# Optimization experiments

Hardware: AMD Instinct MI355X
Metric: run time of the kernel (lower is better)

The kernel has to match this reference:

```python
import jax, jax.numpy as jnp
import numpy as np

B, N, E = 2, 10000, 160000
NODE_DIM, EDGE_DIM, HIDDEN = 128, 64, 256


def setup_inputs() -> dict:
    key = jax.random.key(0)
    ks = jax.random.split(key, 12)
    def lin(k, fan_in, fan_out):
        return jax.random.normal(k, (fan_in, fan_out), dtype=jnp.float32) / np.sqrt(fan_in)
    msg_in = 2 * NODE_DIM + EDGE_DIM   # 320
    upd_in = NODE_DIM + HIDDEN         # 384
    return {
        "node_features": jax.random.normal(ks[0], (B, N, NODE_DIM), dtype=jnp.float32),
        "edge_indices": jax.random.randint(ks[1], (B, E, 2), 0, N, dtype=jnp.int32),
        "edge_features": jax.random.normal(ks[2], (B, E, EDGE_DIM), dtype=jnp.float32),
        "W1m": lin(ks[3], msg_in, HIDDEN),  "b1m": jnp.zeros((HIDDEN,), jnp.float32),
        "W2m": lin(ks[4], HIDDEN, HIDDEN),  "b2m": jnp.zeros((HIDDEN,), jnp.float32),
        "W1u": lin(ks[5], upd_in, HIDDEN),  "b1u": jnp.zeros((HIDDEN,), jnp.float32),
        "W2u": lin(ks[6], HIDDEN, NODE_DIM), "b2u": jnp.zeros((NODE_DIM,), jnp.float32),
    }


def reference(node_features, edge_indices, edge_features,
              W1m, b1m, W2m, b2m, W1u, b1u, W2u, b2u):
    # node_features: [B, N, D]; edge_indices: [B, E, 2]; edge_features: [B, E, F]
    b, n, d = node_features.shape
    e = edge_indices.shape[1]
    src_idx = edge_indices[..., 0]  # [B, E]
    dst_idx = edge_indices[..., 1]  # [B, E]
    # batched gather of endpoint features
    src = jnp.take_along_axis(node_features, src_idx[..., None], axis=1)  # [B, E, D]
    dst = jnp.take_along_axis(node_features, dst_idx[..., None], axis=1)  # [B, E, D]
    msg_in = jnp.concatenate([src, dst, edge_features], axis=-1)          # [B, E, 2D+F]
    h = jax.nn.gelu(jnp.einsum("bei,ih->beh", msg_in, W1m) + b1m)
    messages = jnp.einsum("beh,ho->beo", h, W2m) + b2m                    # [B, E, H]
    # scatter-add into destination node buckets (flatten batch for segment_sum)
    flat_dst = (dst_idx + (jnp.arange(b, dtype=dst_idx.dtype)[:, None] * n)).reshape(-1)
    aggregated = jax.ops.segment_sum(
        messages.reshape(b * e, -1), flat_dst, num_segments=b * n
    ).reshape(b, n, -1)                                                   # [B, N, H]
    upd_in = jnp.concatenate([node_features, aggregated], axis=-1)        # [B, N, D+H]
    u = jax.nn.gelu(jnp.einsum("bni,ih->bnh", upd_in, W1u) + b1u)
    return jnp.einsum("bnh,ho->bno", u, W2u) + b2u                        # [B, N, D]
```

## Files before the change

kernel.cpp:

```cpp
#include <hip/hip_runtime.h>
#include <hip/hip_bf16.h>
#include <math.h>

#define BATCH   2
#define N_NODES 10000
#define E_EDGES 160000
#define BN      (BATCH * N_NODES)
#define BE      (BATCH * E_EDGES)
#define ND      128
#define ED      64
#define HID     256
#define K1      320
#define K2      256
#define K1U     384
#define NOUT    128
#define TMN     32
#define TME     64
#define LDH     264

typedef __attribute__((ext_vector_type(8))) short bf16x8;
typedef __attribute__((ext_vector_type(4))) float f32x4;

__device__ unsigned short g_Pb[(size_t)BN * 512];
__device__ unsigned short g_nodef_bf[(size_t)BN * ND];
__device__ unsigned short g_w1c[HID * K1U];
__device__ unsigned short g_w2ut[K2 * NOUT];
__device__ float          g_bc[HID];
__device__ int            g_hist[BN];

__device__ __forceinline__ float gelu_tanh(float x) {
    float u = 0.7978845608028654f * (x + 0.044715f * x * x * x);
    float e = __expf(2.0f * u);
    float t = 1.0f - 2.0f * __builtin_amdgcn_rcpf(e + 1.0f);
    return 0.5f * x * (1.0f + t);
}

__device__ __forceinline__ unsigned short f2bf(float f) {
    __hip_bfloat16 h = __float2bfloat16(f);
    return *reinterpret_cast<unsigned short*>(&h);
}

__device__ __forceinline__ float bf2f(unsigned short u) {
    unsigned int x = ((unsigned int)u) << 16;
    return *reinterpret_cast<float*>(&x);
}

__global__ __launch_bounds__(256) void prep_all(
    const float* __restrict__ nodef,
    const float* __restrict__ W1m, unsigned short* __restrict__ w1t,
    const float* __restrict__ W1u, const float* __restrict__ W2u,
    const float* __restrict__ W2m, const float* __restrict__ b2m)
{
    int i = blockIdx.x * blockDim.x + threadIdx.x;
    if (i < BN * ND / 4) {
        float4 v = ((const float4*)nodef)[i];
        ushort4 o;
        o.x = f2bf(v.x); o.y = f2bf(v.y); o.z = f2bf(v.z); o.w = f2bf(v.w);
        ((ushort4*)g_nodef_bf)[i] = o;
    }
    if (i < BN) g_hist[i] = 0;
    if (i < K1 * HID) {
        int k = i % K1, n = i / K1;
        w1t[i] = f2bf(W1m[(size_t)k * HID + n]);
    }
    if (i < ND * HID) {
        int k = i % ND, n = i / ND;
        g_w1c[n * K1U + k] = f2bf(W1u[(size_t)k * HID + n]);
    }
    if (i < K2 * NOUT) {
        int k = i % K2, n = i / K2;
        g_w2ut[i] = f2bf(W2u[(size_t)k * NOUT + n]);
    }
    if (i < HID * HID) {
        int n = i & 255;
        int j = i >> 8;
        float a = 0.f;
        #pragma unroll 8
        for (int o = 0; o < HID; ++o)
            a += W2m[(size_t)j * HID + o] * W1u[(size_t)(128 + o) * HID + n];
        g_w1c[n * K1U + 128 + j] = f2bf(a);
    }
    if (i < HID) {
        float c = 0.f;
        #pragma unroll 8
        for (int o = 0; o < HID; ++o)
            c += b2m[o] * W1u[(size_t)(128 + o) * HID + i];
        g_bc[i] = c;
    }
}

__global__ __launch_bounds__(256) void dst_hist(
    const int* __restrict__ eidx, float* __restrict__ agg)
{
    int e = blockIdx.x * blockDim.x + threadIdx.x;
    float4 z = {0.f, 0.f, 0.f, 0.f};
    #pragma unroll
    for (int j = 0; j < 4; ++j)
        ((float4*)agg)[(size_t)j * BE + e] = z;
    if (e < BE) {
        int dst = eidx[2 * e + 1];
        int b   = e / E_EDGES;
        atomicAdd(&g_hist[b * N_NODES + dst], 1);
    }
}

__global__ __launch_bounds__(1024, 1) void scan20k(int* __restrict__ offs)
{
    __shared__ int sh[BN];
    __shared__ int tots[1024];
    const int tid = threadIdx.x;
    for (int j = tid; j < BN; j += 1024) sh[j] = g_hist[j];
    __syncthreads();
    const int base = tid * 20;
    int v[20];
    int s = 0;
    #pragma unroll
    for (int j = 0; j < 20; ++j) {
        int i = base + j;
        int h = (i < BN) ? sh[i] : 0;
        v[j] = s; s += h;
    }
    tots[tid] = s;
    __syncthreads();
    #pragma unroll
    for (int d = 1; d < 1024; d <<= 1) {
        int t = (tid >= d) ? tots[tid - d] : 0;
        __syncthreads();
        tots[tid] += t;
        __syncthreads();
    }
    int excl = tots[tid] - s;
    #pragma unroll
    for (int j = 0; j < 20; ++j) {
        int i = base + j;
        if (i < BN) sh[i] = excl + v[j];
    }
    __syncthreads();
    for (int j = tid; j < BN; j += 1024) offs[j] = sh[j];
}

__global__ __launch_bounds__(512, 2) void pgemm_scatter(
    const unsigned short* __restrict__ w1t,
    const int* __restrict__ eidx,
    int* __restrict__ offs, int* __restrict__ perm)
{
    const int tid  = threadIdx.x;
    {
        int e   = blockIdx.x * 512 + tid;
        int2 se = ((const int2*)eidx)[e];
        int b   = (e >= E_EDGES) ? 1 : 0;
        int pos = atomicAdd(&offs[b * N_NODES + se.y], 1);
        perm[pos] = e;
    }

    const int wave = tid >> 6;
    const int lane = tid & 63;
    const int quad = lane >> 4;
    const int r16  = lane & 15;
    const int n0   = blockIdx.x * TMN;

    const int jb   = (wave & 3) * 64;
    const int koff = (wave < 4) ? 0 : 128;
    const int cb   = (wave < 4) ? 0 : 256;

    f32x4 acc[2][4];
    #pragma unroll
    for (int mt = 0; mt < 2; ++mt)
        #pragma unroll
        for (int nt = 0; nt < 4; ++nt)
            acc[mt][nt] = (f32x4){0.f, 0.f, 0.f, 0.f};

    for (int ks = 0; ks < ND / 32; ++ks) {
        bf16x8 wf[4], nf[2];
        #pragma unroll
        for (int nt = 0; nt < 4; ++nt)
            wf[nt] = *(const bf16x8*)&w1t[(size_t)(jb + nt * 16 + r16) * K1
                                          + koff + ks * 32 + quad * 8];
        #pragma unroll
        for (int mt = 0; mt < 2; ++mt)
            nf[mt] = *(const bf16x8*)&g_nodef_bf[(size_t)(n0 + mt * 16 + r16) * ND
                                                 + ks * 32 + quad * 8];
        #pragma unroll
        for (int mt = 0; mt < 2; ++mt)
            #pragma unroll
            for (int nt = 0; nt < 4; ++nt)
                acc[mt][nt] = __builtin_amdgcn_mfma_f32_16x16x32_bf16(
                    wf[nt], nf[mt], acc[mt][nt], 0, 0, 0);
    }

    #pragma unroll
    for (int nt = 0; nt < 4; ++nt) {
        int j0 = cb + jb + nt * 16 + quad * 4;
        #pragma unroll
        for (int mt = 0; mt < 2; ++mt) {
            int m = n0 + mt * 16 + r16;
            ushort4 o;
            o.x = f2bf(acc[mt][nt][0]); o.y = f2bf(acc[mt][nt][1]);
            o.z = f2bf(acc[mt][nt][2]); o.w = f2bf(acc[mt][nt][3]);
            *(ushort4*)&g_Pb[(size_t)m * 512 + j0] = o;
        }
    }
}

#define EK_SE   0
#define EK_SH   8192
#define EK_SMEM (8192 + TME * LDH * 2)

__global__ __launch_bounds__(512, 6) void edge_mlp_mfma(
    const int*            __restrict__ eidx,
    const float*          __restrict__ edgef,
    const int*            __restrict__ perm,
    const unsigned short* __restrict__ w1t,
    const float*          __restrict__ b1m,
    float* __restrict__ agg)
{
    __shared__ __align__(16) char smem[EK_SMEM];
    unsigned short* sE = (unsigned short*)(smem + EK_SE);
    unsigned short* sH = (unsigned short*)(smem + EK_SH);
    __shared__ int s_src[TME];
    __shared__ int s_dst[TME];
    __shared__ int s_eid[TME];

    const int tid  = threadIdx.x;
    const int wave = tid >> 6;
    const int lane = tid & 63;
    const int quad = lane >> 4;
    const int r16  = lane & 15;
    const int be0  = blockIdx.x * TME;

    if (tid < TME) {
        int eid = perm[be0 + tid];
        int b   = eid / E_EDGES;
        int2 se = ((const int2*)eidx)[eid];
        s_eid[tid] = eid;
        s_src[tid] = b * N_NODES + se.x;
        s_dst[tid] = b * N_NODES + se.y;
    }

    const unsigned short* wB1 = w1t + (size_t)(wave * 32) * K1 + 256;
    bf16x8 wf00 = *(const bf16x8*)&wB1[(size_t)r16        * K1 + quad * 8];
    bf16x8 wf01 = *(const bf16x8*)&wB1[(size_t)r16        * K1 + 32 + quad * 8];
    bf16x8 wf10 = *(const bf16x8*)&wB1[(size_t)(16 + r16) * K1 + quad * 8];
    bf16x8 wf11 = *(const bf16x8*)&wB1[(size_t)(16 + r16) * K1 + 32 + quad * 8];

    __syncthreads();

    {
        int row = tid >> 3;
        int c0  = (tid & 7) * 8;
        const float* fp = edgef + (size_t)s_eid[row] * ED + c0;
        float4 v0 = *(const float4*)fp;
        float4 v1 = *(const float4*)(fp + 4);
        ushort4 o0, o1;
        o0.x = f2bf(v0.x); o0.y = f2bf(v0.y); o0.z = f2bf(v0.z); o0.w = f2bf(v0.w);
        o1.x = f2bf(v1.x); o1.y = f2bf(v1.y); o1.z = f2bf(v1.z); o1.w = f2bf(v1.w);
        int p2 = c0 >> 5, kk = c0 & 31;
        *(ushort4*)&sE[p2 * 2048 + row * 32 + kk]     = o0;
        *(ushort4*)&sE[p2 * 2048 + row * 32 + kk + 4] = o1;
    }
    __syncthreads();

    f32x4 acc[4][2];
    #pragma unroll
    for (int mt = 0; mt < 4; ++mt)
        #pragma unroll
        for (int nt = 0; nt < 2; ++nt)
            acc[mt][nt] = (f32x4){0.f, 0.f, 0.f, 0.f};

    #pragma unroll
    for (int mt = 0; mt < 4; ++mt) {
        bf16x8 e0 = *(const bf16x8*)&sE[(mt * 16 + r16) * 32 + quad * 8];
        bf16x8 e1 = *(const bf16x8*)&sE[2048 + (mt * 16 + r16) * 32 + quad * 8];
        acc[mt][0] = __builtin_amdgcn_mfma_f32_16x16x32_bf16(wf00, e0, acc[mt][0], 0, 0, 0);
        acc[mt][1] = __builtin_amdgcn_mfma_f32_16x16x32_bf16(wf10, e0, acc[mt][1], 0, 0, 0);
        acc[mt][0] = __builtin_amdgcn_mfma_f32_16x16x32_bf16(wf01, e1, acc[mt][0], 0, 0, 0);
        acc[mt][1] = __builtin_amdgcn_mfma_f32_16x16x32_bf16(wf11, e1, acc[mt][1], 0, 0, 0);
    }

    {
        float4 bb[2];
        bb[0] = *(const float4*)&b1m[wave * 32 + quad * 4];
        bb[1] = *(const float4*)&b1m[wave * 32 + 16 + quad * 4];
        #pragma unroll
        for (int mt = 0; mt < 4; ++mt) {
            int m = mt * 16 + r16;
            const unsigned short* pS = &g_Pb[(size_t)s_src[m] * 512];
            const unsigned short* pD = &g_Pb[(size_t)s_dst[m] * 512 + 256];
            #pragma unroll
            for (int nt = 0; nt < 2; ++nt) {
                int n0 = wave * 32 + nt * 16 + quad * 4;
                ushort4 us = *(const ushort4*)(pS + n0);
                ushort4 ud = *(const ushort4*)(pD + n0);
                ushort4 o;
                o.x = f2bf(gelu_tanh(acc[mt][nt][0] + bf2f(us.x) + bf2f(ud.x) + bb[nt].x));
                o.y = f2bf(gelu_tanh(acc[mt][nt][1] + bf2f(us.y) + bf2f(ud.y) + bb[nt].y));
                o.z = f2bf(gelu_tanh(acc[mt][nt][2] + bf2f(us.z) + bf2f(ud.z) + bb[nt].z));
                o.w = f2bf(gelu_tanh(acc[mt][nt][3] + bf2f(us.w) + bf2f(ud.w) + bb[nt].w));
                *(ushort4*)&sH[m * LDH + n0] = o;
            }
        }
    }
    __syncthreads();

    {
        const int cc = tid & 255;
        const int r0 = (tid >> 8) * 32;
        int   cur  = s_dst[r0];
        float racc = 0.f;
        for (int mb = 0; mb < 32; mb += 8) {
            float v[8];
            #pragma unroll
            for (int j = 0; j < 8; ++j)
                v[j] = bf2f(sH[(r0 + mb + j) * LDH + cc]);
            #pragma unroll
            for (int j = 0; j < 8; ++j) {
                int d = s_dst[r0 + mb + j];
                if (d != cur) {
                    atomicAdd(&agg[(size_t)cur * HID + cc], racc);
                    cur = d; racc = v[j];
                } else {
                    racc += v[j];
                }
            }
        }
        atomicAdd(&agg[(size_t)cur * HID + cc], racc);
    }
}

__global__ __launch_bounds__(256, 4) void node_mlp_mfma(
    const float* __restrict__ agg,
    const float* __restrict__ b1u,
    const float* __restrict__ b2u,
    float* __restrict__ out)
{
    __shared__ __align__(16) unsigned short sH[TMN * LDH];

    const int tid  = threadIdx.x;
    const int wave = tid >> 6;
    const int lane = tid & 63;
    const int quad = lane >> 4;
    const int r16  = lane & 15;
    const int n0   = blockIdx.x * TMN;

    f32x4 acc[2][4];
    #pragma unroll
    for (int mt = 0; mt < 2; ++mt)
        #pragma unroll
        for (int nt = 0; nt < 4; ++nt)
            acc[mt][nt] = (f32x4){0.f, 0.f, 0.f, 0.f};

    for (int ks = 0; ks < 4; ++ks) {
        bf16x8 wf[4], nf[2];
        #pragma unroll
        for (int nt = 0; nt < 4; ++nt)
            wf[nt] = *(const bf16x8*)&g_w1c[(size_t)(wave * 64 + nt * 16 + r16) * K1U
                                            + ks * 32 + quad * 8];
        #pragma unroll
        for (int mt = 0; mt < 2; ++mt)
            nf[mt] = *(const bf16x8*)&g_nodef_bf[(size_t)(n0 + mt * 16 + r16) * ND
                                                 + ks * 32 + quad * 8];
        #pragma unroll
        for (int mt = 0; mt < 2; ++mt)
            #pragma unroll
            for (int nt = 0; nt < 4; ++nt)
                acc[mt][nt] = __builtin_amdgcn_mfma_f32_16x16x32_bf16(
                    wf[nt], nf[mt], acc[mt][nt], 0, 0, 0);
    }
    for (int ks = 0; ks < 8; ++ks) {
        bf16x8 wf[4], nf[2];
        #pragma unroll
        for (int nt = 0; nt < 4; ++nt)
            wf[nt] = *(const bf16x8*)&g_w1c[(size_t)(wave * 64 + nt * 16 + r16) * K1U
                                            + (4 + ks) * 32 + quad * 8];
        #pragma unroll
        for (int mt = 0; mt < 2; ++mt) {
            const float* fp = &agg[(size_t)(n0 + mt * 16 + r16) * HID + ks * 32 + quad * 8];
            float4 v0 = *(const float4*)fp;
            float4 v1 = *(const float4*)(fp + 4);
            union { bf16x8 v; ushort4 u[2]; } cv;
            cv.u[0] = (ushort4){f2bf(v0.x), f2bf(v0.y), f2bf(v0.z), f2bf(v0.w)};
            cv.u[1] = (ushort4){f2bf(v1.x), f2bf(v1.y), f2bf(v1.z), f2bf(v1.w)};
            nf[mt] = cv.v;
        }
        #pragma unroll
        for (int mt = 0; mt < 2; ++mt)
            #pragma unroll
            for (int nt = 0; nt < 4; ++nt)
                acc[mt][nt] = __builtin_amdgcn_mfma_f32_16x16x32_bf16(
                    wf[nt], nf[mt], acc[mt][nt], 0, 0, 0);
    }

    #pragma unroll
    for (int nt = 0; nt < 4; ++nt) {
        int nn0 = wave * 64 + nt * 16 + quad * 4;
        float4 bb = *(const float4*)&b1u[nn0];
        float4 bc = *(const float4*)&g_bc[nn0];
        #pragma unroll
        for (int mt = 0; mt < 2; ++mt) {
            int row = n0 + mt * 16 + r16;
            float hv = (float)g_hist[row];
            int m = mt * 16 + r16;
            ushort4 o;
            o.x = f2bf(gelu_tanh(acc[mt][nt][0] + bb.x + hv * bc.x));
            o.y = f2bf(gelu_tanh(acc[mt][nt][1] + bb.y + hv * bc.y));
            o.z = f2bf(gelu_tanh(acc[mt][nt][2] + bb.z + hv * bc.z));
            o.w = f2bf(gelu_tanh(acc[mt][nt][3] + bb.w + hv * bc.w));
            *(ushort4*)&sH[m * LDH + nn0] = o;
        }
    }
    __syncthreads();

    f32x4 acc2[2][2];
    #pragma unroll
    for (int mt = 0; mt < 2; ++mt)
        #pragma unroll
        for (int nt = 0; nt < 2; ++nt)
            acc2[mt][nt] = (f32x4){0.f, 0.f, 0.f, 0.f};

    for (int ks = 0; ks < K2 / 32; ++ks) {
        bf16x8 wf2[2], hf[2];
        #pragma unroll
        for (int nt = 0; nt < 2; ++nt)
            wf2[nt] = *(const bf16x8*)&g_w2ut[(size_t)(wave * 32 + nt * 16 + r16) * K2
                                              + ks * 32 + quad * 8];
        #pragma unroll
        for (int mt = 0; mt < 2; ++mt)
            hf[mt] = *(const bf16x8*)&sH[(mt * 16 + r16) * LDH + ks * 32 + quad * 8];
        #pragma unroll
        for (int mt = 0; mt < 2; ++mt)
            #pragma unroll
            for (int nt = 0; nt < 2; ++nt)
                acc2[mt][nt] = __builtin_amdgcn_mfma_f32_16x16x32_bf16(
                    wf2[nt], hf[mt], acc2[mt][nt], 0, 0, 0);
    }

    #pragma unroll
    for (int nt = 0; nt < 2; ++nt) {
        int j0 = wave * 32 + nt * 16 + quad * 4;
        float4 bb = *(const float4*)&b2u[j0];
        #pragma unroll
        for (int mt = 0; mt < 2; ++mt) {
            int row = n0 + mt * 16 + r16;
            float4 v = {acc2[mt][nt][0] + bb.x, acc2[mt][nt][1] + bb.y,
                        acc2[mt][nt][2] + bb.z, acc2[mt][nt][3] + bb.w};
            *(float4*)&out[(size_t)row * NOUT + j0] = v;
        }
    }
}


extern "C" void kernel_launch(void* const* d_in, const int* in_sizes, int n_in,
                              void* d_out, int out_size, void* d_ws, size_t ws_size,
                              hipStream_t stream) {
    const float* nodef = (const float*)d_in[0];
    const int*   eidx  = (const int*)  d_in[1];
    const float* edgef = (const float*)d_in[2];
    const float* W1m   = (const float*)d_in[3];
    const float* b1m   = (const float*)d_in[4];
    const float* W2m   = (const float*)d_in[5];
    const float* b2m   = (const float*)d_in[6];
    const float* W1u   = (const float*)d_in[7];
    const float* b1u   = (const float*)d_in[8];
    const float* W2u   = (const float*)d_in[9];
    const float* b2u   = (const float*)d_in[10];
    float* out = (float*)d_out;

    char* wsb = (char*)d_ws;
    float* agg = (float*)wsb;

    char* ob = (char*)d_out;
    unsigned short* w1t  = (unsigned short*)(ob + 5120000);
    int* offs            = (int*)(ob + 5494912);
    int* perm            = (int*)(ob + 5574912);

    prep_all<<<(BN * ND / 4 + 255) / 256, 256, 0, stream>>>(
        nodef, W1m, w1t, W1u, W2u, W2m, b2m);

    dst_hist<<<BE / 256, 256, 0, stream>>>(eidx, agg);
    scan20k<<<1, 1024, 0, stream>>>(offs);

    pgemm_scatter<<<BN / TMN, 512, 0, stream>>>(w1t, eidx, offs, perm);

    edge_mlp_mfma<<<BE / TME, 512, 0, stream>>>(
        eidx, edgef, perm, w1t, b1m, agg);

    node_mlp_mfma<<<BN / TMN, 256, 0, stream>>>(agg, b1u, b2u, out);
}
```

Before: 340.3 us.

## Fuse histogram into prep kernel and alias edge-kernel LDS buffers

Result: faster. 331.5 us (-2.6%).

```diff
diff --git a/kernel.cpp b/kernel.cpp
--- a/kernel.cpp
+++ b/kernel.cpp
@@ -27,6 +27,7 @@
 __device__ unsigned short g_w2ut[K2 * NOUT];
 __device__ float          g_bc[HID];
 __device__ int            g_hist[BN];
+__device__ int            g_offs[BN];
 
 __device__ __forceinline__ float gelu_tanh(float x) {
     float u = 0.7978845608028654f * (x + 0.044715f * x * x * x);
@@ -45,20 +46,30 @@
     return *reinterpret_cast<float*>(&x);
 }
 
-__global__ __launch_bounds__(256) void prep_all(
-    const float* __restrict__ nodef,
+__global__ __launch_bounds__(256) void prep_hist(
+    const float* __restrict__ nodef, const int* __restrict__ eidx,
+    float* __restrict__ agg,
     const float* __restrict__ W1m, unsigned short* __restrict__ w1t,
     const float* __restrict__ W1u, const float* __restrict__ W2u,
     const float* __restrict__ W2m, const float* __restrict__ b2m)
 {
     int i = blockIdx.x * blockDim.x + threadIdx.x;
-    if (i < BN * ND / 4) {
+    {
         float4 v = ((const float4*)nodef)[i];
         ushort4 o;
         o.x = f2bf(v.x); o.y = f2bf(v.y); o.z = f2bf(v.z); o.w = f2bf(v.w);
         ((ushort4*)g_nodef_bf)[i] = o;
     }
-    if (i < BN) g_hist[i] = 0;
+    {
+        float4 z = {0.f, 0.f, 0.f, 0.f};
+        ((float4*)agg)[i] = z;
+        ((float4*)agg)[i + 640000] = z;
+    }
+    if (i < BE) {
+        int dst = eidx[2 * i + 1];
+        int b   = i / E_EDGES;
+        atomicAdd(&g_hist[b * N_NODES + dst], 1);
+    }
     if (i < K1 * HID) {
         int k = i % K1, n = i / K1;
         w1t[i] = f2bf(W1m[(size_t)k * HID + n]);
@@ -89,27 +100,15 @@
     }
 }
 
-__global__ __launch_bounds__(256) void dst_hist(
-    const int* __restrict__ eidx, float* __restrict__ agg)
-{
-    int e = blockIdx.x * blockDim.x + threadIdx.x;
-    float4 z = {0.f, 0.f, 0.f, 0.f};
-    #pragma unroll
-    for (int j = 0; j < 4; ++j)
-        ((float4*)agg)[(size_t)j * BE + e] = z;
-    if (e < BE) {
-        int dst = eidx[2 * e + 1];
-        int b   = e / E_EDGES;
-        atomicAdd(&g_hist[b * N_NODES + dst], 1);
-    }
-}
-
-__global__ __launch_bounds__(1024, 1) void scan20k(int* __restrict__ offs)
+__global__ __launch_bounds__(1024, 1) void scan20k()
 {
     __shared__ int sh[BN];
     __shared__ int tots[1024];
     const int tid = threadIdx.x;
-    for (int j = tid; j < BN; j += 1024) sh[j] = g_hist[j];
+    for (int j = tid; j < BN; j += 1024) {
+        sh[j] = g_hist[j];
+        g_hist[j] = 0;
+    }
     __syncthreads();
     const int base = tid * 20;
     int v[20];
@@ -136,20 +135,20 @@
         if (i < BN) sh[i] = excl + v[j];
     }
     __syncthreads();
-    for (int j = tid; j < BN; j += 1024) offs[j] = sh[j];
+    for (int j = tid; j < BN; j += 1024) g_offs[j] = sh[j];
 }
 
 __global__ __launch_bounds__(512, 2) void pgemm_scatter(
     const unsigned short* __restrict__ w1t,
     const int* __restrict__ eidx,
-    int* __restrict__ offs, int* __restrict__ perm)
+    int* __restrict__ perm)
 {
     const int tid  = threadIdx.x;
     {
         int e   = blockIdx.x * 512 + tid;
         int2 se = ((const int2*)eidx)[e];
         int b   = (e >= E_EDGES) ? 1 : 0;
-        int pos = atomicAdd(&offs[b * N_NODES + se.y], 1);
+        int pos = atomicAdd(&g_offs[b * N_NODES + se.y], 1);
         perm[pos] = e;
     }
 
@@ -202,11 +201,9 @@
     }
 }
 
-#define EK_SE   0
-#define EK_SH   8192
-#define EK_SMEM (8192 + TME * LDH * 2)
-
-__global__ __launch_bounds__(512, 6) void edge_mlp_mfma(
+#define EK_SMEM (TME * LDH * 2)
+
+__global__ __launch_bounds__(512, 8) void edge_mlp_mfma(
     const int*            __restrict__ eidx,
     const float*          __restrict__ edgef,
     const int*            __restrict__ perm,
@@ -215,8 +212,8 @@
     float* __restrict__ agg)
 {
     __shared__ __align__(16) char smem[EK_SMEM];
-    unsigned short* sE = (unsigned short*)(smem + EK_SE);
-    unsigned short* sH = (unsigned short*)(smem + EK_SH);
+    unsigned short* sE = (unsigned short*)smem;
+    unsigned short* sH = (unsigned short*)smem;
     __shared__ int s_src[TME];
     __shared__ int s_dst[TME];
     __shared__ int s_eid[TME];
@@ -242,6 +239,8 @@
     bf16x8 wf01 = *(const bf16x8*)&wB1[(size_t)r16        * K1 + 32 + quad * 8];
     bf16x8 wf10 = *(const bf16x8*)&wB1[(size_t)(16 + r16) * K1 + quad * 8];
     bf16x8 wf11 = *(const bf16x8*)&wB1[(size_t)(16 + r16) * K1 + 32 + quad * 8];
+    float4 bb0 = *(const float4*)&b1m[wave * 32 + quad * 4];
+    float4 bb1 = *(const float4*)&b1m[wave * 32 + 16 + quad * 4];
 
     __syncthreads();
 
@@ -276,28 +275,25 @@
         acc[mt][0] = __builtin_amdgcn_mfma_f32_16x16x32_bf16(wf01, e1, acc[mt][0], 0, 0, 0);
         acc[mt][1] = __builtin_amdgcn_mfma_f32_16x16x32_bf16(wf11, e1, acc[mt][1], 0, 0, 0);
     }
-
-    {
-        float4 bb[2];
-        bb[0] = *(const float4*)&b1m[wave * 32 + quad * 4];
-        bb[1] = *(const float4*)&b1m[wave * 32 + 16 + quad * 4];
-        #pragma unroll
-        for (int mt = 0; mt < 4; ++mt) {
-            int m = mt * 16 + r16;
-            const unsigned short* pS = &g_Pb[(size_t)s_src[m] * 512];
-            const unsigned short* pD = &g_Pb[(size_t)s_dst[m] * 512 + 256];
-            #pragma unroll
-            for (int nt = 0; nt < 2; ++nt) {
-                int n0 = wave * 32 + nt * 16 + quad * 4;
-                ushort4 us = *(const ushort4*)(pS + n0);
-                ushort4 ud = *(const ushort4*)(pD + n0);
-                ushort4 o;
-                o.x = f2bf(gelu_tanh(acc[mt][nt][0] + bf2f(us.x) + bf2f(ud.x) + bb[nt].x));
-                o.y = f2bf(gelu_tanh(acc[mt][nt][1] + bf2f(us.y) + bf2f(ud.y) + bb[nt].y));
-                o.z = f2bf(gelu_tanh(acc[mt][nt][2] + bf2f(us.z) + bf2f(ud.z) + bb[nt].z));
-                o.w = f2bf(gelu_tanh(acc[mt][nt][3] + bf2f(us.w) + bf2f(ud.w) + bb[nt].w));
-                *(ushort4*)&sH[m * LDH + n0] = o;
-            }
+    __syncthreads();
+
+    #pragma unroll
+    for (int mt = 0; mt < 4; ++mt) {
+        int m = mt * 16 + r16;
+        const unsigned short* pS = &g_Pb[(size_t)s_src[m] * 512];
+        const unsigned short* pD = &g_Pb[(size_t)s_dst[m] * 512 + 256];
+        #pragma unroll
+        for (int nt = 0; nt < 2; ++nt) {
+            int n0 = wave * 32 + nt * 16 + quad * 4;
+            float4 bb = nt ? bb1 : bb0;
+            ushort4 us = *(const ushort4*)(pS + n0);
+            ushort4 ud = *(const ushort4*)(pD + n0);
+            ushort4 o;
+            o.x = f2bf(gelu_tanh(acc[mt][nt][0] + bf2f(us.x) + bf2f(ud.x) + bb.x));
+            o.y = f2bf(gelu_tanh(acc[mt][nt][1] + bf2f(us.y) + bf2f(ud.y) + bb.y));
+            o.z = f2bf(gelu_tanh(acc[mt][nt][2] + bf2f(us.z) + bf2f(ud.z) + bb.z));
+            o.w = f2bf(gelu_tanh(acc[mt][nt][3] + bf2f(us.w) + bf2f(ud.w) + bb.w));
+            *(ushort4*)&sH[m * LDH + n0] = o;
         }
     }
     __syncthreads();
@@ -397,8 +393,10 @@
         float4 bc = *(const float4*)&g_bc[nn0];
         #pragma unroll
         for (int mt = 0; mt < 2; ++mt) {
-            int row = n0 + mt * 16 + r16;
-            float hv = (float)g_hist[row];
+            int row  = n0 + mt * 16 + r16;
+            int incl = g_offs[row];
+            int prev = (row > 0) ? g_offs[row - 1] : 0;
+            float hv = (float)(incl - prev);
             int m = mt * 16 + r16;
             ushort4 o;
             o.x = f2bf(gelu_tanh(acc[mt][nt][0] + bb.x + hv * bc.x));
@@ -470,16 +468,14 @@
 
     char* ob = (char*)d_out;
     unsigned short* w1t  = (unsigned short*)(ob + 5120000);
-    int* offs            = (int*)(ob + 5494912);
     int* perm            = (int*)(ob + 5574912);
 
-    prep_all<<<(BN * ND / 4 + 255) / 256, 256, 0, stream>>>(
-        nodef, W1m, w1t, W1u, W2u, W2m, b2m);
-
-    dst_hist<<<BE / 256, 256, 0, stream>>>(eidx, agg);
-    scan20k<<<1, 1024, 0, stream>>>(offs);
-
-    pgemm_scatter<<<BN / TMN, 512, 0, stream>>>(w1t, eidx, offs, perm);
+    prep_hist<<<BN * ND / 4 / 256, 256, 0, stream>>>(
+        nodef, eidx, agg, W1m, w1t, W1u, W2u, W2m, b2m);
+
+    scan20k<<<1, 1024, 0, stream>>>();
+
+    pgemm_scatter<<<BN / TMN, 512, 0, stream>>>(w1t, eidx, perm);
 
     edge_mlp_mfma<<<BE / TME, 512, 0, stream>>>(
         eidx, edgef, perm, w1t, b1m, agg);
```
